# Performance work log

Measured on AMD Instinct MI355X. Metric: run time of the kernel, lower is better.

## Reference

```python
import jax, jax.numpy as jnp
import numpy as np

H = 4096          # hidden_dim
VOCAB = 4         # vocab_size
MAX_LEN = 52      # max_len
PAD = 3           # pad_token_id
BLOCK = 12        # pad inserted after every 12 generated tokens
N_STEPS = 48      # loop breaks after 48 GRU steps (48 tokens + 4 pads = 52)


def setup_inputs() -> dict:
    key = jax.random.key(0)
    ks = jax.random.split(key, 9)
    s = 1.0 / np.sqrt(H)  # PyTorch default uniform init bound
    u = lambda k, shape: jax.random.uniform(k, shape, jnp.float32, -s, s)
    return {
        "tensor_state": jax.random.normal(ks[0], (1, H), jnp.float32),
        "token_embedding": jax.random.normal(ks[1], (VOCAB, H), jnp.float32),
        "pos_embedding": jax.random.normal(ks[2], (1, MAX_LEN, H), jnp.float32),
        "W_ih": u(ks[3], (3 * H, H)),
        "W_hh": u(ks[4], (3 * H, H)),
        "b_ih": u(ks[5], (3 * H,)),
        "b_hh": u(ks[6], (3 * H,)),
        "W_out": u(ks[7], (VOCAB, H)),
        "b_out": u(ks[8], (VOCAB,)),
    }


def reference(tensor_state, token_embedding, pos_embedding,
              W_ih, W_hh, b_ih, b_hh, W_out, b_out):
    def gru_cell(x, h):  # x, h: (1, H); PyTorch gate order [r, z, n]
        gi = x @ W_ih.T + b_ih
        gh = h @ W_hh.T + b_hh
        i_r, i_z, i_n = jnp.split(gi, 3, axis=-1)
        h_r, h_z, h_n = jnp.split(gh, 3, axis=-1)
        r = jax.nn.sigmoid(i_r + h_r)
        z = jax.nn.sigmoid(i_z + h_z)
        n = jnp.tanh(i_n + r * h_n)
        return (1.0 - z) * n + z * h

    def step(carry, step_idx):
        h, tok = carry
        x = token_embedding[tok][None, :] + pos_embedding[0, step_idx][None, :]
        h = gru_cell(x, h)
        logits = h @ W_out.T + b_out            # (1, VOCAB)
        nxt = jnp.argmax(logits[0]).astype(jnp.int32)
        # after every 12th step the next input is forced to PAD
        nxt_in = jnp.where((step_idx + 1) % BLOCK == 0, jnp.int32(PAD), nxt)
        return (h, nxt_in), nxt

    init = (tensor_state, jnp.int32(PAD))
    _, toks = jax.lax.scan(step, init, jnp.arange(N_STEPS))  # (48,)
    # interleave a PAD token after each block of 12 generated tokens
    toks = toks.reshape(N_STEPS // BLOCK, BLOCK)             # (4, 12)
    pads = jnp.full((N_STEPS // BLOCK, 1), PAD, toks.dtype)
    out = jnp.concatenate([toks, pads], axis=1).reshape(-1)[:MAX_LEN]
    return out[None, :]  # (1, 52) int32 token ids
```

## Files before the change

kernel.cpp:

```cpp
#include <hip/hip_runtime.h>
#include <hip/hip_fp16.h>
#include <cmath>

#define H     4096
#define H3    12288
#define NSTEPS 48
#define PAD_TOK 3
#define NBLK  2048
#define SLOTG 64
#define FPSCALE 4294967296.0f
#define INVSCALE 2.3283064365386963e-10f

#define QSCALE     8128.0f
#define INV_QSCALE (1.0f / 8128.0f)

typedef _Float16 flt16;
typedef flt16 flt16x8 __attribute__((ext_vector_type(8)));
typedef float f32x4    __attribute__((ext_vector_type(4)));

__device__ inline long long shfl_xor_ll(long long v, int mask) {
    int2 p = *(int2*)&v;
    p.x = __shfl_xor(p.x, mask, 64);
    p.y = __shfl_xor(p.y, mask, 64);
    return *(long long*)&p;
}

__global__ __launch_bounds__(256)
void startup1_kernel(const float* __restrict__ emb, const float* __restrict__ pos,
                     flt16* __restrict__ X16, unsigned long long* __restrict__ slots,
                     int* __restrict__ out) {
    const int bid = blockIdx.x, tid = threadIdx.x;
    if (bid < 64) {
        const int r = bid;
        for (int k4 = tid; k4 < H / 4; k4 += 256) {
            float4 v = {0.f, 0.f, 0.f, 0.f};
            if (r < 4)       v = *(const float4*)(emb + (size_t)r * H + k4 * 4);
            else if (r < 52) v = *(const float4*)(pos + (size_t)(r - 4) * H + k4 * 4);
            flt16 o[4] = {(flt16)v.x, (flt16)v.y, (flt16)v.z, (flt16)v.w};
            *(float2*)(X16 + (size_t)r * H + k4 * 4) = *(float2*)o;
        }
    } else if (bid < 72) {
        for (int idx = (bid - 64) * 256 + tid; idx < NSTEPS * SLOTG * 4; idx += 8 * 256)
            slots[idx] = 0ull;
    } else if (tid == 0) {
        out[12] = PAD_TOK; out[25] = PAD_TOK; out[38] = PAD_TOK; out[51] = PAD_TOK;
    }
}

__global__ __launch_bounds__(256)
void precompute_kernel(const flt16* __restrict__ X16, const float* __restrict__ W_ih,
                       const float* __restrict__ b_ih, float* __restrict__ G) {
    __shared__ f32x4 red[4][4][64];
    const int tid  = threadIdx.x;
    const int kq   = tid >> 6;
    const int lane = tid & 63;
    const int jcol = blockIdx.x * 16 + (lane & 15);
    const int kgrp = (lane >> 4) * 8;
    const int mrow = lane & 15;

    const float* wbase = W_ih + (size_t)jcol * H + kq * 1024 + kgrp;
    const flt16* xbase = X16 + kq * 1024 + kgrp;

    const f32x4 z = {0.f, 0.f, 0.f, 0.f};
    f32x4 acc[4] = {z, z, z, z};

    #pragma unroll 2
    for (int ks = 0; ks < 32; ++ks) {
        const int k = ks * 32;
        float4 wlo = *(const float4*)(wbase + k);
        float4 whi = *(const float4*)(wbase + k + 4);
        flt16x8 b;
        b[0] = (flt16)wlo.x; b[1] = (flt16)wlo.y; b[2] = (flt16)wlo.z; b[3] = (flt16)wlo.w;
        b[4] = (flt16)whi.x; b[5] = (flt16)whi.y; b[6] = (flt16)whi.z; b[7] = (flt16)whi.w;
        #pragma unroll
        for (int mt = 0; mt < 4; ++mt) {
            flt16x8 a = *(const flt16x8*)(xbase + (size_t)(mt * 16 + mrow) * H + k);
            acc[mt] = __builtin_amdgcn_mfma_f32_16x16x32_f16(a, b, acc[mt], 0, 0, 0);
        }
    }

    #pragma unroll
    for (int mt = 0; mt < 4; ++mt) red[kq][mt][lane] = acc[mt];
    __syncthreads();

    f32x4 tot = red[0][kq][lane];
    #pragma unroll
    for (int q = 1; q < 4; ++q) tot = tot + red[q][kq][lane];
    const float bj = b_ih[jcol];
    #pragma unroll
    for (int e = 0; e < 4; ++e) {
        const int r = kq * 16 + (lane >> 4) * 4 + e;
        if (r < 52) G[(size_t)r * H3 + jcol] = tot[e] + (r >= 4 ? bj : 0.f);
    }
}

__global__ __launch_bounds__(256)
void step0_kernel(const float* __restrict__ Wh, signed char* __restrict__ Wq,
                  const float* __restrict__ b_hh, const float* __restrict__ G,
                  const float* __restrict__ W_out, const float* __restrict__ b_out,
                  const float* __restrict__ h_old, float* __restrict__ h_new,
                  unsigned long long* __restrict__ slots_out) {
    __shared__ float red2[12];
    const int tid = threadIdx.x, wave = tid >> 6, lane = tid & 63;
    const int i0 = blockIdx.x * 2;
    const int kh = wave & 1;
    const int rg = wave >> 1;

    float acc[3] = {0.f, 0.f, 0.f};
    const float* rp[3];
    signed char* wq[3];
    #pragma unroll
    for (int m = 0; m < 3; ++m) {
        const int rr = rg * 3 + m;
        const int j  = (rr >> 1) * H + i0 + (rr & 1);
        rp[m] = Wh + (size_t)j * H + kh * 2048;
        wq[m] = Wq + (size_t)j * H + kh * 2048;
    }
    const float* hbase = h_old + kh * 2048;

    #pragma unroll
    for (int it = 0; it < 4; ++it) {
        const int kb = it * 512 + lane * 8;
        float4 xa = *(const float4*)(hbase + kb);
        float4 xb = *(const float4*)(hbase + kb + 4);
        #pragma unroll
        for (int m = 0; m < 3; ++m) {
            float4 wa = *(const float4*)(rp[m] + kb);
            float4 wb = *(const float4*)(rp[m] + kb + 4);
            acc[m] += wa.x * xa.x + wa.y * xa.y + wa.z * xa.z + wa.w * xa.w
                    + wb.x * xb.x + wb.y * xb.y + wb.z * xb.z + wb.w * xb.w;
            int q0 = __float2int_rn(wa.x * QSCALE) & 255;
            int q1 = __float2int_rn(wa.y * QSCALE) & 255;
            int q2 = __float2int_rn(wa.z * QSCALE) & 255;
            int q3 = __float2int_rn(wa.w * QSCALE) & 255;
            int q4 = __float2int_rn(wb.x * QSCALE) & 255;
            int q5 = __float2int_rn(wb.y * QSCALE) & 255;
            int q6 = __float2int_rn(wb.z * QSCALE) & 255;
            int q7 = __float2int_rn(wb.w * QSCALE) & 255;
            uint2 o;
            o.x = (unsigned)(q0 | (q1 << 8) | (q2 << 16) | (q3 << 24));
            o.y = (unsigned)(q4 | (q5 << 8) | (q6 << 16) | (q7 << 24));
            *(uint2*)(wq[m] + kb) = o;
        }
    }

    #pragma unroll
    for (int m = 0; m < 3; ++m) {
        float s = acc[m];
        for (int off = 32; off; off >>= 1) s += __shfl_xor(s, off, 64);
        if (lane == 0) red2[(rg * 3 + m) * 2 + kh] = s;
    }
    __syncthreads();

    if (tid < 2) {
        const int i = i0 + tid;
        const float* gE = G + (size_t)PAD_TOK * H3;
        const float* gP = G + (size_t)4 * H3;
        float vr = red2[(0 + tid) * 2] + red2[(0 + tid) * 2 + 1] + b_hh[i];
        float vz = red2[(2 + tid) * 2] + red2[(2 + tid) * 2 + 1] + b_hh[H + i];
        float vn = red2[(4 + tid) * 2] + red2[(4 + tid) * 2 + 1] + b_hh[2 * H + i];
        float gir = gE[i]         + gP[i];
        float giz = gE[H + i]     + gP[H + i];
        float gin = gE[2 * H + i] + gP[2 * H + i];
        float r = 1.f / (1.f + expf(-(gir + vr)));
        float z = 1.f / (1.f + expf(-(giz + vz)));
        float n = tanhf(gin + r * vn);
        float hn = (1.f - z) * n + z * h_old[i];
        h_new[i] = hn;

        float p0 = W_out[i] * hn;
        float p1 = W_out[H + i] * hn;
        float p2 = W_out[2 * H + i] * hn;
        float p3 = W_out[3 * H + i] * hn;
        p0 += __shfl_xor(p0, 1, 64); p1 += __shfl_xor(p1, 1, 64);
        p2 += __shfl_xor(p2, 1, 64); p3 += __shfl_xor(p3, 1, 64);
        if (tid == 0) {
            unsigned long long* so = slots_out + (size_t)(blockIdx.x & (SLOTG - 1)) * 4;
            atomicAdd(&so[0], (unsigned long long)(long long)llrintf(p0 * FPSCALE));
            atomicAdd(&so[1], (unsigned long long)(long long)llrintf(p1 * FPSCALE));
            atomicAdd(&so[2], (unsigned long long)(long long)llrintf(p2 * FPSCALE));
            atomicAdd(&so[3], (unsigned long long)(long long)llrintf(p3 * FPSCALE));
        }
    }
}

__global__ __launch_bounds__(256)
void stepq_kernel(const signed char* __restrict__ Wq, const float* __restrict__ b_hh,
                  const float* __restrict__ G, const float* __restrict__ W_out,
                  const float* __restrict__ b_out,
                  const float* __restrict__ h_old, float* __restrict__ h_new,
                  const unsigned long long* __restrict__ slots_in,
                  unsigned long long* __restrict__ slots_out,
                  int* __restrict__ out, int t) {
    __shared__ float red2[12];
    const int tid = threadIdx.x, wave = tid >> 6, lane = tid & 63;
    const int i0 = blockIdx.x * 2;
    const int kh = wave & 1;
    const int rg = wave >> 1;

    float acc[3] = {0.f, 0.f, 0.f};
    const signed char* rp[3];
    #pragma unroll
    for (int m = 0; m < 3; ++m) {
        const int rr = rg * 3 + m;
        const int j  = (rr >> 1) * H + i0 + (rr & 1);
        rp[m] = Wq + (size_t)j * H + kh * 2048;
    }
    const float* hbase = h_old + kh * 2048;

    #pragma unroll
    for (int it = 0; it < 4; ++it) {
        const int kb = it * 512 + lane * 8;
        float4 xa = *(const float4*)(hbase + kb);
        float4 xb = *(const float4*)(hbase + kb + 4);
        #pragma unroll
        for (int m = 0; m < 3; ++m) {
            uint2 u = *(const uint2*)(rp[m] + kb);
            const int ux = (int)u.x, uy = (int)u.y;
            float w0 = (float)((ux << 24) >> 24);
            float w1 = (float)((ux << 16) >> 24);
            float w2 = (float)((ux <<  8) >> 24);
            float w3 = (float)( ux        >> 24);
            float w4 = (float)((uy << 24) >> 24);
            float w5 = (float)((uy << 16) >> 24);
            float w6 = (float)((uy <<  8) >> 24);
            float w7 = (float)( uy        >> 24);
            acc[m] += w0 * xa.x + w1 * xa.y + w2 * xa.z + w3 * xa.w
                    + w4 * xb.x + w5 * xb.y + w6 * xb.z + w7 * xb.w;
        }
    }

    #pragma unroll
    for (int m = 0; m < 3; ++m) {
        float s = acc[m];
        for (int off = 32; off; off >>= 1) s += __shfl_xor(s, off, 64);
        if (lane == 0) red2[(rg * 3 + m) * 2 + kh] = s * INV_QSCALE;
    }

    int tok = PAD_TOK;
    if (wave == 0 && t > 0) {
        const long long* sp = (const long long*)(slots_in + (size_t)lane * 4);
        long long a0 = sp[0], a1 = sp[1], a2 = sp[2], a3 = sp[3];
        #pragma unroll
        for (int off = 32; off; off >>= 1) {
            a0 += shfl_xor_ll(a0, off); a1 += shfl_xor_ll(a1, off);
            a2 += shfl_xor_ll(a2, off); a3 += shfl_xor_ll(a3, off);
        }
        float lg[4] = {(float)a0 * INVSCALE + b_out[0], (float)a1 * INVSCALE + b_out[1],
                       (float)a2 * INVSCALE + b_out[2], (float)a3 * INVSCALE + b_out[3]};
        int best = 0;
        #pragma unroll
        for (int v = 1; v < 4; ++v) if (lg[v] > lg[best]) best = v;
        if (blockIdx.x == 0 && tid == 0)
            out[((t - 1) / 12) * 13 + ((t - 1) % 12)] = best;
        tok = (t % 12 == 0) ? PAD_TOK : best;
    }
    __syncthreads();

    if (tid < 2) {
        const int i = i0 + tid;
        const float* gE = G + (size_t)tok * H3;
        const float* gP = G + (size_t)(4 + t) * H3;
        float vr = red2[(0 + tid) * 2] + red2[(0 + tid) * 2 + 1] + b_hh[i];
        float vz = red2[(2 + tid) * 2] + red2[(2 + tid) * 2 + 1] + b_hh[H + i];
        float vn = red2[(4 + tid) * 2] + red2[(4 + tid) * 2 + 1] + b_hh[2 * H + i];
        float gir = gE[i]         + gP[i];
        float giz = gE[H + i]     + gP[H + i];
        float gin = gE[2 * H + i] + gP[2 * H + i];
        float r = 1.f / (1.f + expf(-(gir + vr)));
        float z = 1.f / (1.f + expf(-(giz + vz)));
        float n = tanhf(gin + r * vn);
        float hn = (1.f - z) * n + z * h_old[i];
        h_new[i] = hn;

        float p0 = W_out[i] * hn;
        float p1 = W_out[H + i] * hn;
        float p2 = W_out[2 * H + i] * hn;
        float p3 = W_out[3 * H + i] * hn;
        p0 += __shfl_xor(p0, 1, 64); p1 += __shfl_xor(p1, 1, 64);
        p2 += __shfl_xor(p2, 1, 64); p3 += __shfl_xor(p3, 1, 64);
        if (tid == 0) {
            unsigned long long* so = slots_out + (size_t)(blockIdx.x & (SLOTG - 1)) * 4;
            atomicAdd(&so[0], (unsigned long long)(long long)llrintf(p0 * FPSCALE));
            atomicAdd(&so[1], (unsigned long long)(long long)llrintf(p1 * FPSCALE));
            atomicAdd(&so[2], (unsigned long long)(long long)llrintf(p2 * FPSCALE));
            atomicAdd(&so[3], (unsigned long long)(long long)llrintf(p3 * FPSCALE));
        }
    }
}

__global__ __launch_bounds__(256)
void stepf_kernel(const float* __restrict__ Wh, const float* __restrict__ b_hh,
                  const float* __restrict__ G, const float* __restrict__ W_out,
                  const float* __restrict__ b_out,
                  const float* __restrict__ h_old, float* __restrict__ h_new,
                  const unsigned long long* __restrict__ slots_in,
                  unsigned long long* __restrict__ slots_out,
                  int* __restrict__ out, int t) {
    __shared__ float red2[12];
    const int tid = threadIdx.x, wave = tid >> 6, lane = tid & 63;
    const int i0 = blockIdx.x * 2;
    const int kh = wave & 1;
    const int rg = wave >> 1;

    float acc[3] = {0.f, 0.f, 0.f};
    const float* rp[3];
    #pragma unroll
    for (int m = 0; m < 3; ++m) {
        const int rr = rg * 3 + m;
        const int j  = (rr >> 1) * H + i0 + (rr & 1);
        rp[m] = Wh + (size_t)j * H + kh * 2048;
    }
    const float* hbase = h_old + kh * 2048;

    #pragma unroll
    for (int it = 0; it < 8; ++it) {
        const int kb = it * 256 + lane * 4;
        float4 x = *(const float4*)(hbase + kb);
        #pragma unroll
        for (int m = 0; m < 3; ++m) {
            float4 w = *(const float4*)(rp[m] + kb);
            acc[m] += w.x * x.x + w.y * x.y + w.z * x.z + w.w * x.w;
        }
    }

    #pragma unroll
    for (int m = 0; m < 3; ++m) {
        float s = acc[m];
        for (int off = 32; off; off >>= 1) s += __shfl_xor(s, off, 64);
        if (lane == 0) red2[(rg * 3 + m) * 2 + kh] = s;
    }

    int tok = PAD_TOK;
    if (wave == 0 && t > 0) {
        const long long* sp = (const long long*)(slots_in + (size_t)lane * 4);
        long long a0 = sp[0], a1 = sp[1], a2 = sp[2], a3 = sp[3];
        #pragma unroll
        for (int off = 32; off; off >>= 1) {
            a0 += shfl_xor_ll(a0, off); a1 += shfl_xor_ll(a1, off);
            a2 += shfl_xor_ll(a2, off); a3 += shfl_xor_ll(a3, off);
        }
        float lg[4] = {(float)a0 * INVSCALE + b_out[0], (float)a1 * INVSCALE + b_out[1],
                       (float)a2 * INVSCALE + b_out[2], (float)a3 * INVSCALE + b_out[3]};
        int best = 0;
        #pragma unroll
        for (int v = 1; v < 4; ++v) if (lg[v] > lg[best]) best = v;
        if (blockIdx.x == 0 && tid == 0)
            out[((t - 1) / 12) * 13 + ((t - 1) % 12)] = best;
        tok = (t % 12 == 0) ? PAD_TOK : best;
    }
    __syncthreads();

    if (tid < 2) {
        const int i = i0 + tid;
        const float* gE = G + (size_t)tok * H3;
        const float* gP = G + (size_t)(4 + t) * H3;
        float vr = red2[(0 + tid) * 2] + red2[(0 + tid) * 2 + 1] + b_hh[i];
        float vz = red2[(2 + tid) * 2] + red2[(2 + tid) * 2 + 1] + b_hh[H + i];
        float vn = red2[(4 + tid) * 2] + red2[(4 + tid) * 2 + 1] + b_hh[2 * H + i];
        float gir = gE[i]         + gP[i];
        float giz = gE[H + i]     + gP[H + i];
        float gin = gE[2 * H + i] + gP[2 * H + i];
        float r = 1.f / (1.f + expf(-(gir + vr)));
        float z = 1.f / (1.f + expf(-(giz + vz)));
        float n = tanhf(gin + r * vn);
        float hn = (1.f - z) * n + z * h_old[i];
        h_new[i] = hn;

        float p0 = W_out[i] * hn;
        float p1 = W_out[H + i] * hn;
        float p2 = W_out[2 * H + i] * hn;
        float p3 = W_out[3 * H + i] * hn;
        p0 += __shfl_xor(p0, 1, 64); p1 += __shfl_xor(p1, 1, 64);
        p2 += __shfl_xor(p2, 1, 64); p3 += __shfl_xor(p3, 1, 64);
        if (tid == 0) {
            unsigned long long* so = slots_out + (size_t)(blockIdx.x & (SLOTG - 1)) * 4;
            atomicAdd(&so[0], (unsigned long long)(long long)llrintf(p0 * FPSCALE));
            atomicAdd(&so[1], (unsigned long long)(long long)llrintf(p1 * FPSCALE));
            atomicAdd(&so[2], (unsigned long long)(long long)llrintf(p2 * FPSCALE));
            atomicAdd(&so[3], (unsigned long long)(long long)llrintf(p3 * FPSCALE));
        }
    }
}

__global__ __launch_bounds__(64)
void final_kernel(const unsigned long long* __restrict__ slots,
                  const float* __restrict__ b_out, int* __restrict__ out) {
    const int lane = threadIdx.x;
    const long long* sp = (const long long*)(slots + (size_t)lane * 4);
    long long a0 = sp[0], a1 = sp[1], a2 = sp[2], a3 = sp[3];
    #pragma unroll
    for (int off = 32; off; off >>= 1) {
        a0 += shfl_xor_ll(a0, off); a1 += shfl_xor_ll(a1, off);
        a2 += shfl_xor_ll(a2, off); a3 += shfl_xor_ll(a3, off);
    }
    if (lane == 0) {
        float lg[4] = {(float)a0 * INVSCALE + b_out[0], (float)a1 * INVSCALE + b_out[1],
                       (float)a2 * INVSCALE + b_out[2], (float)a3 * INVSCALE + b_out[3]};
        int best = 0;
        for (int v = 1; v < 4; ++v) if (lg[v] > lg[best]) best = v;
        out[(47 / 12) * 13 + (47 % 12)] = best;
    }
}

extern "C" void kernel_launch(void* const* d_in, const int* in_sizes, int n_in,
                              void* d_out, int out_size, void* d_ws, size_t ws_size,
                              hipStream_t stream) {
    const float* ts    = (const float*)d_in[0];
    const float* emb   = (const float*)d_in[1];
    const float* pos   = (const float*)d_in[2];
    const float* W_ih  = (const float*)d_in[3];
    const float* W_hh  = (const float*)d_in[4];
    const float* b_ih  = (const float*)d_in[5];
    const float* b_hh  = (const float*)d_in[6];
    const float* W_out = (const float*)d_in[7];
    const float* b_out = (const float*)d_in[8];
    int* out = (int*)d_out;

    const size_t wq_bytes   = (size_t)H3 * H;
    const size_t x16_bytes  = (size_t)64 * H * 2;
    const size_t slot_bytes = (size_t)NSTEPS * SLOTG * 4 * 8;
    const size_t rest_bytes = (size_t)52 * H3 * 4 + 2 * H * 4 + slot_bytes + x16_bytes;
    const bool use_q = ws_size >= wq_bytes + rest_bytes + 256;

    char* wp = (char*)d_ws;
    signed char* Wq = nullptr;
    if (use_q) { Wq = (signed char*)wp; wp += wq_bytes; }
    flt16* X16 = (flt16*)wp; wp += x16_bytes;
    float* G   = (float*)wp; wp += (size_t)52 * H3 * 4;
    float* hA  = (float*)wp; wp += H * 4;
    float* hB  = (float*)wp; wp += H * 4;
    unsigned long long* slots = (unsigned long long*)wp;

    hipLaunchKernelGGL(startup1_kernel, dim3(73), dim3(256), 0, stream,
                       emb, pos, X16, slots, out);
    hipLaunchKernelGGL(precompute_kernel, dim3(768), dim3(256), 0, stream,
                       X16, W_ih, b_ih, G);

    if (use_q) {
        hipLaunchKernelGGL(step0_kernel, dim3(NBLK), dim3(256), 0, stream,
                           W_hh, Wq, b_hh, G, W_out, b_out, ts, hA,
                           slots );
        for (int t = 1; t < NSTEPS; ++t) {
            const float* ho = (t & 1) ? hA : hB;
            float*       hn = (t & 1) ? hB : hA;
            const unsigned long long* si = slots + (size_t)(t - 1) * SLOTG * 4;
            unsigned long long*       so = slots + (size_t)t * SLOTG * 4;
            hipLaunchKernelGGL(stepq_kernel, dim3(NBLK), dim3(256), 0, stream,
                               Wq, b_hh, G, W_out, b_out, ho, hn, si, so, out, t);
        }
    } else {
        for (int t = 0; t < NSTEPS; ++t) {
            const float* ho = (t == 0) ? ts : ((t & 1) ? hA : hB);
            float*       hn = (t & 1) ? hB : hA;
            const unsigned long long* si = slots + (size_t)(t > 0 ? t - 1 : 0) * SLOTG * 4;
            unsigned long long*       so = slots + (size_t)t * SLOTG * 4;
            hipLaunchKernelGGL(stepf_kernel, dim3(NBLK), dim3(256), 0, stream,
                               W_hh, b_hh, G, W_out, b_out, ho, hn, si, so, out, t);
        }
    }
    hipLaunchKernelGGL(final_kernel, dim3(1), dim3(64), 0, stream,
                       slots + (size_t)(NSTEPS - 1) * SLOTG * 4, b_out, out);
}
```

Measured before the change: 783.8 us.

## Restructure int8 GRU step kernel to four hidden units per block with batched loads

The quantized step kernel now assigns four hidden units per block (1024 blocks) with each wave covering full rows, so there is no K split across waves. All h and weight loads are issued up front as 16-byte vectors before the dot products, which exposes more memory-level parallelism. Halving the block count cuts per-block overhead such as the slot reduction and the atomics. The cost is higher register pressure from holding 16 float4 and 12 uint4 values per thread, and fewer blocks in flight.

```diff
diff --git a/kernel.cpp b/kernel.cpp
--- a/kernel.cpp
+++ b/kernel.cpp
@@ -6,7 +6,8 @@
 #define H3    12288
 #define NSTEPS 48
 #define PAD_TOK 3
-#define NBLK  2048
+#define NBLK0 2048
+#define NBLKQ 1024
 #define SLOTG 64
 #define FPSCALE 4294967296.0f
 #define INVSCALE 2.3283064365386963e-10f
@@ -23,6 +24,11 @@
     p.x = __shfl_xor(p.x, mask, 64);
     p.y = __shfl_xor(p.y, mask, 64);
     return *(long long*)&p;
+}
+
+__device__ inline float dotd(int ud, float4 x) {
+    return (float)((ud << 24) >> 24) * x.x + (float)((ud << 16) >> 24) * x.y
+         + (float)((ud <<  8) >> 24) * x.z + (float)( ud        >> 24) * x.w;
 }
 
 __global__ __launch_bounds__(256)
@@ -194,39 +200,135 @@
                   int* __restrict__ out, int t) {
     __shared__ float red2[12];
     const int tid = threadIdx.x, wave = tid >> 6, lane = tid & 63;
+    const int i0 = blockIdx.x * 4;
+
+    const signed char* rp[3];
+    #pragma unroll
+    for (int m = 0; m < 3; ++m) {
+        const int rr = wave * 3 + m;
+        rp[m] = Wq + (size_t)((rr >> 2) * H + i0 + (rr & 3)) * H;
+    }
+
+    float4 hv[16];
+    #pragma unroll
+    for (int it = 0; it < 4; ++it)
+        #pragma unroll
+        for (int c = 0; c < 4; ++c)
+            hv[it * 4 + c] = *(const float4*)(h_old + it * 1024 + lane * 16 + c * 4);
+
+    uint4 wv0[4], wv1[4], wv2[4];
+    #pragma unroll
+    for (int it = 0; it < 4; ++it) {
+        wv0[it] = *(const uint4*)(rp[0] + it * 1024 + lane * 16);
+        wv1[it] = *(const uint4*)(rp[1] + it * 1024 + lane * 16);
+        wv2[it] = *(const uint4*)(rp[2] + it * 1024 + lane * 16);
+    }
+
+    float acc[3] = {0.f, 0.f, 0.f};
+    #pragma unroll
+    for (int it = 0; it < 4; ++it) {
+        acc[0] += dotd((int)wv0[it].x, hv[it * 4 + 0]) + dotd((int)wv0[it].y, hv[it * 4 + 1])
+                + dotd((int)wv0[it].z, hv[it * 4 + 2]) + dotd((int)wv0[it].w, hv[it * 4 + 3]);
+        acc[1] += dotd((int)wv1[it].x, hv[it * 4 + 0]) + dotd((int)wv1[it].y, hv[it * 4 + 1])
+                + dotd((int)wv1[it].z, hv[it * 4 + 2]) + dotd((int)wv1[it].w, hv[it * 4 + 3]);
+        acc[2] += dotd((int)wv2[it].x, hv[it * 4 + 0]) + dotd((int)wv2[it].y, hv[it * 4 + 1])
+                + dotd((int)wv2[it].z, hv[it * 4 + 2]) + dotd((int)wv2[it].w, hv[it * 4 + 3]);
+    }
+
+    #pragma unroll
+    for (int m = 0; m < 3; ++m) {
+        float s = acc[m];
+        for (int off = 32; off; off >>= 1) s += __shfl_xor(s, off, 64);
+        if (lane == 0) red2[wave * 3 + m] = s * INV_QSCALE;
+    }
+
+    int tok = PAD_TOK;
+    if (wave == 0 && t > 0) {
+        const long long* sp = (const long long*)(slots_in + (size_t)lane * 4);
+        long long a0 = sp[0], a1 = sp[1], a2 = sp[2], a3 = sp[3];
+        #pragma unroll
+        for (int off = 32; off; off >>= 1) {
+            a0 += shfl_xor_ll(a0, off); a1 += shfl_xor_ll(a1, off);
+            a2 += shfl_xor_ll(a2, off); a3 += shfl_xor_ll(a3, off);
+        }
+        float lg[4] = {(float)a0 * INVSCALE + b_out[0], (float)a1 * INVSCALE + b_out[1],
+                       (float)a2 * INVSCALE + b_out[2], (float)a3 * INVSCALE + b_out[3]};
+        int best = 0;
+        #pragma unroll
+        for (int v = 1; v < 4; ++v) if (lg[v] > lg[best]) best = v;
+        if (blockIdx.x == 0 && tid == 0)
+            out[((t - 1) / 12) * 13 + ((t - 1) % 12)] = best;
+        tok = (t % 12 == 0) ? PAD_TOK : best;
+    }
+    __syncthreads();
+
+    if (tid < 4) {
+        const int i = i0 + tid;
+        const float* gE = G + (size_t)tok * H3;
+        const float* gP = G + (size_t)(4 + t) * H3;
+        float vr = red2[0 + tid] + b_hh[i];
+        float vz = red2[4 + tid] + b_hh[H + i];
+        float vn = red2[8 + tid] + b_hh[2 * H + i];
+        float gir = gE[i]         + gP[i];
+        float giz = gE[H + i]     + gP[H + i];
+        float gin = gE[2 * H + i] + gP[2 * H + i];
+        float r = 1.f / (1.f + expf(-(gir + vr)));
+        float z = 1.f / (1.f + expf(-(giz + vz)));
+        float n = tanhf(gin + r * vn);
+        float hn = (1.f - z) * n + z * h_old[i];
+        h_new[i] = hn;
+
+        float p0 = W_out[i] * hn;
+        float p1 = W_out[H + i] * hn;
+        float p2 = W_out[2 * H + i] * hn;
+        float p3 = W_out[3 * H + i] * hn;
+        #pragma unroll
+        for (int off = 2; off; off >>= 1) {
+            p0 += __shfl_xor(p0, off, 64); p1 += __shfl_xor(p1, off, 64);
+            p2 += __shfl_xor(p2, off, 64); p3 += __shfl_xor(p3, off, 64);
+        }
+        if (tid == 0) {
+            unsigned long long* so = slots_out + (size_t)(blockIdx.x & (SLOTG - 1)) * 4;
+            atomicAdd(&so[0], (unsigned long long)(long long)llrintf(p0 * FPSCALE));
+            atomicAdd(&so[1], (unsigned long long)(long long)llrintf(p1 * FPSCALE));
+            atomicAdd(&so[2], (unsigned long long)(long long)llrintf(p2 * FPSCALE));
+            atomicAdd(&so[3], (unsigned long long)(long long)llrintf(p3 * FPSCALE));
+        }
+    }
+}
+
+__global__ __launch_bounds__(256)
+void stepf_kernel(const float* __restrict__ Wh, const float* __restrict__ b_hh,
+                  const float* __restrict__ G, const float* __restrict__ W_out,
+                  const float* __restrict__ b_out,
+                  const float* __restrict__ h_old, float* __restrict__ h_new,
+                  const unsigned long long* __restrict__ slots_in,
+                  unsigned long long* __restrict__ slots_out,
+                  int* __restrict__ out, int t) {
+    __shared__ float red2[12];
+    const int tid = threadIdx.x, wave = tid >> 6, lane = tid & 63;
     const int i0 = blockIdx.x * 2;
     const int kh = wave & 1;
     const int rg = wave >> 1;
 
     float acc[3] = {0.f, 0.f, 0.f};
-    const signed char* rp[3];
+    const float* rp[3];
     #pragma unroll
     for (int m = 0; m < 3; ++m) {
         const int rr = rg * 3 + m;
         const int j  = (rr >> 1) * H + i0 + (rr & 1);
-        rp[m] = Wq + (size_t)j * H + kh * 2048;
+        rp[m] = Wh + (size_t)j * H + kh * 2048;
     }
     const float* hbase = h_old + kh * 2048;
 
     #pragma unroll
-    for (int it = 0; it < 4; ++it) {
-        const int kb = it * 512 + lane * 8;
-        float4 xa = *(const float4*)(hbase + kb);
-        float4 xb = *(const float4*)(hbase + kb + 4);
+    for (int it = 0; it < 8; ++it) {
+        const int kb = it * 256 + lane * 4;
+        float4 x = *(const float4*)(hbase + kb);
         #pragma unroll
         for (int m = 0; m < 3; ++m) {
-            uint2 u = *(const uint2*)(rp[m] + kb);
-            const int ux = (int)u.x, uy = (int)u.y;
-            float w0 = (float)((ux << 24) >> 24);
-            float w1 = (float)((ux << 16) >> 24);
-            float w2 = (float)((ux <<  8) >> 24);
-            float w3 = (float)( ux        >> 24);
-            float w4 = (float)((uy << 24) >> 24);
-            float w5 = (float)((uy << 16) >> 24);
-            float w6 = (float)((uy <<  8) >> 24);
-            float w7 = (float)( uy        >> 24);
-            acc[m] += w0 * xa.x + w1 * xa.y + w2 * xa.z + w3 * xa.w
-                    + w4 * xb.x + w5 * xb.y + w6 * xb.z + w7 * xb.w;
+            float4 w = *(const float4*)(rp[m] + kb);
+            acc[m] += w.x * x.x + w.y * x.y + w.z * x.z + w.w * x.w;
         }
     }
 
@@ -234,7 +336,7 @@
     for (int m = 0; m < 3; ++m) {
         float s = acc[m];
         for (int off = 32; off; off >>= 1) s += __shfl_xor(s, off, 64);
-        if (lane == 0) red2[(rg * 3 + m) * 2 + kh] = s * INV_QSCALE;
+        if (lane == 0) red2[(rg * 3 + m) * 2 + kh] = s;
     }
 
     int tok = PAD_TOK;
@@ -289,100 +391,6 @@
     }
 }
 
-__global__ __launch_bounds__(256)
-void stepf_kernel(const float* __restrict__ Wh, const float* __restrict__ b_hh,
-                  const float* __restrict__ G, const float* __restrict__ W_out,
-                  const float* __restrict__ b_out,
-                  const float* __restrict__ h_old, float* __restrict__ h_new,
-                  const unsigned long long* __restrict__ slots_in,
-                  unsigned long long* __restrict__ slots_out,
-                  int* __restrict__ out, int t) {
-    __shared__ float red2[12];
-    const int tid = threadIdx.x, wave = tid >> 6, lane = tid & 63;
-    const int i0 = blockIdx.x * 2;
-    const int kh = wave & 1;
-    const int rg = wave >> 1;
-
-    float acc[3] = {0.f, 0.f, 0.f};
-    const float* rp[3];
-    #pragma unroll
-    for (int m = 0; m < 3; ++m) {
-        const int rr = rg * 3 + m;
-        const int j  = (rr >> 1) * H + i0 + (rr & 1);
-        rp[m] = Wh + (size_t)j * H + kh * 2048;
-    }
-    const float* hbase = h_old + kh * 2048;
-
-    #pragma unroll
-    for (int it = 0; it < 8; ++it) {
-        const int kb = it * 256 + lane * 4;
-        float4 x = *(const float4*)(hbase + kb);
-        #pragma unroll
-        for (int m = 0; m < 3; ++m) {
-            float4 w = *(const float4*)(rp[m] + kb);
-            acc[m] += w.x * x.x + w.y * x.y + w.z * x.z + w.w * x.w;
-        }
-    }
-
-    #pragma unroll
-    for (int m = 0; m < 3; ++m) {
-        float s = acc[m];
-        for (int off = 32; off; off >>= 1) s += __shfl_xor(s, off, 64);
-        if (lane == 0) red2[(rg * 3 + m) * 2 + kh] = s;
-    }
-
-    int tok = PAD_TOK;
-    if (wave == 0 && t > 0) {
-        const long long* sp = (const long long*)(slots_in + (size_t)lane * 4);
-        long long a0 = sp[0], a1 = sp[1], a2 = sp[2], a3 = sp[3];
-        #pragma unroll
-        for (int off = 32; off; off >>= 1) {
-            a0 += shfl_xor_ll(a0, off); a1 += shfl_xor_ll(a1, off);
-            a2 += shfl_xor_ll(a2, off); a3 += shfl_xor_ll(a3, off);
-        }
-        float lg[4] = {(float)a0 * INVSCALE + b_out[0], (float)a1 * INVSCALE + b_out[1],
-                       (float)a2 * INVSCALE + b_out[2], (float)a3 * INVSCALE + b_out[3]};
-        int best = 0;
-        #pragma unroll
-        for (int v = 1; v < 4; ++v) if (lg[v] > lg[best]) best = v;
-        if (blockIdx.x == 0 && tid == 0)
-            out[((t - 1) / 12) * 13 + ((t - 1) % 12)] = best;
-        tok = (t % 12 == 0) ? PAD_TOK : best;
-    }
-    __syncthreads();
-
-    if (tid < 2) {
-        const int i = i0 + tid;
-        const float* gE = G + (size_t)tok * H3;
-        const float* gP = G + (size_t)(4 + t) * H3;
-        float vr = red2[(0 + tid) * 2] + red2[(0 + tid) * 2 + 1] + b_hh[i];
-        float vz = red2[(2 + tid) * 2] + red2[(2 + tid) * 2 + 1] + b_hh[H + i];
-        float vn = red2[(4 + tid) * 2] + red2[(4 + tid) * 2 + 1] + b_hh[2 * H + i];
-        float gir = gE[i]         + gP[i];
-        float giz = gE[H + i]     + gP[H + i];
-        float gin = gE[2 * H + i] + gP[2 * H + i];
-        float r = 1.f / (1.f + expf(-(gir + vr)));
-        float z = 1.f / (1.f + expf(-(giz + vz)));
-        float n = tanhf(gin + r * vn);
-        float hn = (1.f - z) * n + z * h_old[i];
-        h_new[i] = hn;
-
-        float p0 = W_out[i] * hn;
-        float p1 = W_out[H + i] * hn;
-        float p2 = W_out[2 * H + i] * hn;
-        float p3 = W_out[3 * H + i] * hn;
-        p0 += __shfl_xor(p0, 1, 64); p1 += __shfl_xor(p1, 1, 64);
-        p2 += __shfl_xor(p2, 1, 64); p3 += __shfl_xor(p3, 1, 64);
-        if (tid == 0) {
-            unsigned long long* so = slots_out + (size_t)(blockIdx.x & (SLOTG - 1)) * 4;
-            atomicAdd(&so[0], (unsigned long long)(long long)llrintf(p0 * FPSCALE));
-            atomicAdd(&so[1], (unsigned long long)(long long)llrintf(p1 * FPSCALE));
-            atomicAdd(&so[2], (unsigned long long)(long long)llrintf(p2 * FPSCALE));
-            atomicAdd(&so[3], (unsigned long long)(long long)llrintf(p3 * FPSCALE));
-        }
-    }
-}
-
 __global__ __launch_bounds__(64)
 void final_kernel(const unsigned long long* __restrict__ slots,
                   const float* __restrict__ b_out, int* __restrict__ out) {
@@ -438,7 +446,7 @@
                        X16, W_ih, b_ih, G);
 
     if (use_q) {
-        hipLaunchKernelGGL(step0_kernel, dim3(NBLK), dim3(256), 0, stream,
+        hipLaunchKernelGGL(step0_kernel, dim3(NBLK0), dim3(256), 0, stream,
                            W_hh, Wq, b_hh, G, W_out, b_out, ts, hA,
                            slots );
         for (int t = 1; t < NSTEPS; ++t) {
@@ -446,7 +454,7 @@
             float*       hn = (t & 1) ? hB : hA;
             const unsigned long long* si = slots + (size_t)(t - 1) * SLOTG * 4;
             unsigned long long*       so = slots + (size_t)t * SLOTG * 4;
-            hipLaunchKernelGGL(stepq_kernel, dim3(NBLK), dim3(256), 0, stream,
+            hipLaunchKernelGGL(stepq_kernel, dim3(NBLKQ), dim3(256), 0, stream,
                                Wq, b_hh, G, W_out, b_out, ho, hn, si, so, out, t);
         }
     } else {
@@ -455,7 +463,7 @@
             float*       hn = (t & 1) ? hB : hA;
             const unsigned long long* si = slots + (size_t)(t > 0 ? t - 1 : 0) * SLOTG * 4;
             unsigned long long*       so = slots + (size_t)t * SLOTG * 4;
-            hipLaunchKernelGGL(stepf_kernel, dim3(NBLK), dim3(256), 0, stream,
+            hipLaunchKernelGGL(stepf_kernel, dim3(NBLK0), dim3(256), 0, stream,
                                W_hh, b_hh, G, W_out, b_out, ho, hn, si, so, out, t);
         }
     }
```

Result: faster. 740.3 us (-5.5%).
